# Optimization experiments

Hardware: AMD Instinct MI355X
Metric: run time of the kernel (lower is better)

## Reference

```python
import jax, jax.numpy as jnp
import numpy as np

T, B, I, H = 512, 64, 256, 256
ACT_EXP2 = 7   # activation scale = 2^-7
W_EXP2 = 8     # weight scale = 2^-8
QMIN, QMAX = -128.0, 127.0  # int8 symmetric, zp=0


def fq(x, exp2_inv):
    """Fake-quantize (round/clamp/dequant) with straight-through estimator."""
    scale = 2.0 ** (-exp2_inv)
    y = jnp.clip(jnp.round(x / scale), QMIN, QMAX) * scale
    return x + jax.lax.stop_gradient(y - x)


def setup_inputs() -> dict:
    key = jax.random.key(0)
    k = jax.random.split(key, 5)
    x = jax.random.normal(k[0], (T, B, I), jnp.float32)
    h0 = jnp.zeros((B, H), jnp.float32)
    W = jax.random.normal(k[1], (I, 3 * H), jnp.float32) / np.sqrt(I)
    R = jax.random.normal(k[2], (H, 3 * H), jnp.float32) / np.sqrt(H)
    bx = jax.random.normal(k[3], (3 * H,), jnp.float32) * 0.1
    br = jax.random.normal(k[4], (3 * H,), jnp.float32) * 0.1
    return {"x": x, "h0": h0, "W": W, "R": R, "bx": bx, "br": br}


def gru_quant(x, h0, W, R, bx, br):
    # quantize weights/biases once (weight.W / weight.R / weight.bx / weight.br)
    Wq = fq(W, W_EXP2)
    Rq = fq(R, W_EXP2)
    bxq = fq(bx, W_EXP2)
    brq = fq(br, W_EXP2)
    # hoisted input matmul: Wx = fq(fq(x) @ Wq)  -> [T, B, 3H]
    Wx = fq(jnp.einsum('tbi,ij->tbj', fq(x, ACT_EXP2), Wq), ACT_EXP2)
    Hh = h0.shape[-1]
    bz, brg, bg = bxq[:Hh], bxq[Hh:2 * Hh], bxq[2 * Hh:]

    def step(h, wx_t):
        hq = fq(h, ACT_EXP2)                      # input.h
        Rh = fq(hq @ Rq, ACT_EXP2)                # matmul.Rh
        v = fq(Rh + brq, ACT_EXP2)                # op.Rh_add_br
        wz, wr, wg = wx_t[:, :Hh], wx_t[:, Hh:2 * Hh], wx_t[:, 2 * Hh:]
        vz, vr, vg = v[:, :Hh], v[:, Hh:2 * Hh], v[:, 2 * Hh:]
        z = fq(jax.nn.sigmoid(fq(wz + bz + vz, ACT_EXP2)), ACT_EXP2)  # gate.z
        r = fq(jax.nn.sigmoid(fq(wr + brg + vr, ACT_EXP2)), ACT_EXP2)  # gate.r
        rRh = fq(r * vg, ACT_EXP2)                # op.rRh
        g = fq(jnp.tanh(fq(wg + bg + rRh, ACT_EXP2)), ACT_EXP2)        # gate.g
        old = fq(z * h, ACT_EXP2)                 # op.old_contrib
        new = fq((1.0 - z) * g, ACT_EXP2)         # op.new_contrib
        h_new = old + new
        return h_new, h_new

    _, hs = jax.lax.scan(step, h0, Wx)  # hs: [T, B, H]
    return hs


def reference(x, h0, W, R, bx, br):
    return gru_quant(x, h0, W, R, bx, br)
```

## Files before the change

### kernel.cpp

```cpp
#include <hip/hip_runtime.h>
#include <hip/hip_bf16.h>
#include <stdint.h>


#define T_STEPS 512
#define BATCH   64
#define IDIM    256
#define HDIM    256
#define N3H     768

#if defined(__has_builtin)
#if __has_builtin(__builtin_amdgcn_sdot4)
#define DOT4(a,b,c) __builtin_amdgcn_sdot4((int)(a),(int)(b),(int)(c),false)
#endif
#endif
#ifndef DOT4
__device__ __forceinline__ int dot4_sw(uint32_t a, uint32_t b, int c){
  c += (int)(int8_t)(a)      * (int)(int8_t)(b);
  c += (int)(int8_t)(a>>8)   * (int)(int8_t)(b>>8);
  c += (int)(int8_t)(a>>16)  * (int)(int8_t)(b>>16);
  c += (int)(int8_t)(a>>24)  * (int)(int8_t)(b>>24);
  return c;
}
#define DOT4(a,b,c) dot4_sw((uint32_t)(a),(uint32_t)(b),(int)(c))
#endif

#define CHUNK(W,c) (((c)&3)==0 ? W[(c)>>2].x : ((c)&3)==1 ? W[(c)>>2].y : \
                    ((c)&3)==2 ? W[(c)>>2].z : W[(c)>>2].w)

__device__ __forceinline__ int rneclamp(float v) {
  int q = (int)rintf(v);
  return min(127, max(-128, q));
}

__device__ __forceinline__ uint32_t packq4(float4 f, float sc) {
  uint32_t b0 = (uint32_t)(uint8_t)(int8_t)rneclamp(f.x * sc);
  uint32_t b1 = (uint32_t)(uint8_t)(int8_t)rneclamp(f.y * sc);
  uint32_t b2 = (uint32_t)(uint8_t)(int8_t)rneclamp(f.z * sc);
  uint32_t b3 = (uint32_t)(uint8_t)(int8_t)rneclamp(f.w * sc);
  return b0 | (b1 << 8) | (b2 << 16) | (b3 << 24);
}

__global__ void prep_kernel(const float* __restrict__ W, const float* __restrict__ R,
                            const float* __restrict__ bx, const float* __restrict__ br,
                            int8_t* __restrict__ Wq, int8_t* __restrict__ Rq,
                            int8_t* __restrict__ bx8, int8_t* __restrict__ br8) {
  const int NW = IDIM * N3H;
  int idx = blockIdx.x * 256 + threadIdx.x;
  if (idx < NW) {
    int k = idx / N3H, j = idx % N3H;
    Wq[((size_t)(k >> 4) * N3H + j) * 16 + (k & 15)] = (int8_t)rneclamp(W[idx] * 256.0f);
  } else if (idx < 2 * NW) {
    int i2 = idx - NW;
    int k = i2 / N3H, j = i2 % N3H;
    Rq[((size_t)(k >> 4) * N3H + j) * 16 + (k & 15)] = (int8_t)rneclamp(R[i2] * 256.0f);
  } else if (idx < 2 * NW + N3H) {
    int i2 = idx - 2 * NW;
    bx8[i2] = (int8_t)rneclamp(bx[i2] * 256.0f);
  } else if (idx < 2 * NW + 2 * N3H) {
    int i2 = idx - 2 * NW - N3H;
    br8[i2] = (int8_t)rneclamp(br[i2] * 256.0f);
  }
}

__global__ __launch_bounds__(768, 1) void gemm_wx_kernel(
    const float* __restrict__ x, const int8_t* __restrict__ Wq,
    int8_t* __restrict__ WxQ8) {
  const int t = blockIdx.x;
  const int j = threadIdx.x;

  __shared__ uint4 xq4[64 * 16];
  uint32_t* xq = (uint32_t*)xq4;

  uint4 w[16];
  const uint4* wp = (const uint4*)Wq;
  #pragma unroll
  for (int kk = 0; kk < 16; ++kk) w[kk] = wp[kk * N3H + j];

  const float4* xg = (const float4*)(x) + (size_t)t * 4096;
  for (int i = j; i < 4096; i += 768) {
    float4 f = xg[i];
    xq[i] = packq4(f, 128.0f);
  }
  __syncthreads();

  for (int r = 0; r < 64; ++r) {
    int s = 0;
    #pragma unroll
    for (int kk = 0; kk < 16; ++kk) {
      uint4 hv = xq4[r * 16 + kk];
      s = DOT4(hv.x, w[kk].x, s);
      s = DOT4(hv.y, w[kk].y, s);
      s = DOT4(hv.z, w[kk].z, s);
      s = DOT4(hv.w, w[kk].w, s);
    }
    int q = rneclamp((float)s * (1.0f / 256.0f));
    WxQ8[((size_t)r * T_STEPS + t) * N3H + j] = (int8_t)q;
  }
}

__global__ __launch_bounds__(256, 1) void gru_rec2_kernel(
    const float* __restrict__ h0, const int8_t* __restrict__ Rq,
    const int8_t* __restrict__ bx8, const int8_t* __restrict__ br8,
    const int8_t* __restrict__ WxQ8, float* __restrict__ out) {
  const int b = blockIdx.x;
  const int j = threadIdx.x;
  const int lane = j & 63;

  __shared__ uint32_t hq[2][64];
  __shared__ int8_t lutS[256];
  __shared__ int8_t lutT[256];

  uint4 wz[16], wr[16], wg[16];
  const uint4* rp = (const uint4*)Rq;
  #pragma unroll
  for (int kk = 0; kk < 16; ++kk) {
    wz[kk] = rp[kk * N3H + j];
    wr[kk] = rp[kk * N3H + 256 + j];
    wg[kk] = rp[kk * N3H + 512 + j];
  }
  const int bz  = (int)bx8[j];
  const int brg = (int)bx8[j + 256];
  const int bg  = (int)bx8[j + 512];
  const int vbz = (int)br8[j];
  const int vbr = (int)br8[j + 256];
  const int vbg = (int)br8[j + 512];

  {
    double a = ((double)j - 128.0) / 128.0;
    lutS[j] = (int8_t)min(127, max(-128, (int)rint(128.0 / (1.0 + exp(-a)))));
    lutT[j] = (int8_t)min(127, max(-128, (int)rint(128.0 * tanh(a))));
  }
  float hf = h0[b * HDIM + j];
  ((int8_t*)&hq[0][0])[j] = (int8_t)rneclamp(hf * 128.0f);
  __syncthreads();

  const int8_t* wxp = WxQ8 + (size_t)b * T_STEPS * N3H + j;
  float* outp = out + (size_t)b * HDIM + j;

  int wxz = (int)wxp[0];
  int wxr = (int)wxp[256];
  int wxg = (int)wxp[512];

  for (int t = 0; t < T_STEPS; ++t) {
    const int cur = t & 1, nxt = cur ^ 1;
    int nz = 0, nr = 0, ng = 0;
    if (t + 1 < T_STEPS) {
      const int8_t* p = wxp + (size_t)(t + 1) * N3H;
      nz = (int)p[0]; nr = (int)p[256]; ng = (int)p[512];
    }

    uint32_t hw = hq[cur][lane];
    int sz = 0, sr = 0, sg = 0;
    #pragma unroll
    for (int c = 0; c < 64; ++c) {
      int hc = __builtin_amdgcn_readlane((int)hw, c);
      sz = DOT4(hc, CHUNK(wz, c), sz);
      sr = DOT4(hc, CHUNK(wr, c), sr);
      sg = DOT4(hc, CHUNK(wg, c), sg);
    }
    int Rz = rneclamp((float)sz * (1.0f / 256.0f));
    int Rr = rneclamp((float)sr * (1.0f / 256.0f));
    int Rg = rneclamp((float)sg * (1.0f / 256.0f));
    int vz = rneclamp((float)(2 * Rz + vbz) * 0.5f);
    int vr = rneclamp((float)(2 * Rr + vbr) * 0.5f);
    int vg = rneclamp((float)(2 * Rg + vbg) * 0.5f);

    int az = rneclamp((float)(2 * wxz + bz + 2 * vz) * 0.5f);
    int zi = (int)lutS[az + 128];
    int ar = rneclamp((float)(2 * wxr + brg + 2 * vr) * 0.5f);
    int ri = (int)lutS[ar + 128];
    int rrh = rneclamp((float)(ri * vg) * (1.0f / 128.0f));
    int ag = rneclamp((float)(2 * wxg + bg + 2 * rrh) * 0.5f);
    int gi = (int)lutT[ag + 128];
    int oldi = rneclamp((float)zi * hf);
    int newi = rneclamp((float)((128 - zi) * gi) * (1.0f / 128.0f));
    int hi = oldi + newi;
    hf = (float)hi * (1.0f / 128.0f);
    outp[(size_t)t * BATCH * HDIM] = hf;
    ((int8_t*)&hq[nxt][0])[j] = (int8_t)min(127, max(-128, hi));
    __syncthreads();

    wxz = nz; wxr = nr; wxg = ng;
  }
}

extern "C" void kernel_launch(void* const* d_in, const int* in_sizes, int n_in,
                              void* d_out, int out_size, void* d_ws, size_t ws_size,
                              hipStream_t stream) {
  const float* x  = (const float*)d_in[0];
  const float* h0 = (const float*)d_in[1];
  const float* W  = (const float*)d_in[2];
  const float* R  = (const float*)d_in[3];
  const float* bx = (const float*)d_in[4];
  const float* br = (const float*)d_in[5];
  float* out = (float*)d_out;

  const size_t NW = (size_t)IDIM * N3H;
  int8_t* Wq  = (int8_t*)d_ws;
  int8_t* Rq  = Wq + NW;
  int8_t* bx8 = Rq + NW;
  int8_t* br8 = bx8 + N3H;
  int8_t* WxQ8 = br8 + N3H;

  {
    int total = (int)(2 * NW + 2 * N3H);
    int blocks = (total + 255) / 256;
    prep_kernel<<<blocks, 256, 0, stream>>>(W, R, bx, br, Wq, Rq, bx8, br8);
  }
  gemm_wx_kernel<<<T_STEPS, 768, 0, stream>>>(x, Wq, WxQ8);
  gru_rec2_kernel<<<BATCH, 256, 0, stream>>>(h0, Rq, bx8, br8, WxQ8, out);
}
```

Before: 488.8 us.

## Split recurrent matvec K dimension across two thread halves with shared-memory reduction

```diff
diff --git a/kernel.cpp b/kernel.cpp
--- a/kernel.cpp
+++ b/kernel.cpp
@@ -53,7 +53,7 @@
   } else if (idx < 2 * NW) {
     int i2 = idx - NW;
     int k = i2 / N3H, j = i2 % N3H;
-    Rq[((size_t)(k >> 4) * N3H + j) * 16 + (k & 15)] = (int8_t)rneclamp(R[i2] * 256.0f);
+    Rq[(size_t)j * HDIM + k] = (int8_t)rneclamp(R[i2] * 256.0f);
   } else if (idx < 2 * NW + N3H) {
     int i2 = idx - 2 * NW;
     bx8[i2] = (int8_t)rneclamp(bx[i2] * 256.0f);
@@ -99,89 +99,100 @@
   }
 }
 
-__global__ __launch_bounds__(256, 1) void gru_rec2_kernel(
+__global__ __launch_bounds__(512, 2) void gru_rec3_kernel(
     const float* __restrict__ h0, const int8_t* __restrict__ Rq,
     const int8_t* __restrict__ bx8, const int8_t* __restrict__ br8,
     const int8_t* __restrict__ WxQ8, float* __restrict__ out) {
-  const int b = blockIdx.x;
-  const int j = threadIdx.x;
-  const int lane = j & 63;
+  const int b    = blockIdx.x;
+  const int tid  = threadIdx.x;
+  const int lane = tid & 63;
+  const int half = tid >> 8;
+  const int j    = tid & 255;
 
   __shared__ uint32_t hq[2][64];
+  __shared__ int part[N3H];
   __shared__ int8_t lutS[256];
   __shared__ int8_t lutT[256];
 
-  uint4 wz[16], wr[16], wg[16];
-  const uint4* rp = (const uint4*)Rq;
-  #pragma unroll
-  for (int kk = 0; kk < 16; ++kk) {
-    wz[kk] = rp[kk * N3H + j];
-    wr[kk] = rp[kk * N3H + 256 + j];
-    wg[kk] = rp[kk * N3H + 512 + j];
-  }
-  const int bz  = (int)bx8[j];
-  const int brg = (int)bx8[j + 256];
-  const int bg  = (int)bx8[j + 512];
-  const int vbz = (int)br8[j];
-  const int vbr = (int)br8[j + 256];
-  const int vbg = (int)br8[j + 512];
-
+  uint4 wz[8], wr[8], wg[8];
   {
+    const uint4* pz = (const uint4*)(Rq + (size_t)j * HDIM)         + half * 8;
+    const uint4* pr = (const uint4*)(Rq + (size_t)(j + 256) * HDIM) + half * 8;
+    const uint4* pg = (const uint4*)(Rq + (size_t)(j + 512) * HDIM) + half * 8;
+    #pragma unroll
+    for (int kk = 0; kk < 8; ++kk) { wz[kk] = pz[kk]; wr[kk] = pr[kk]; wg[kk] = pg[kk]; }
+  }
+
+  float hf = 0.0f;
+  int bz = 0, brg = 0, bg = 0, vbz = 0, vbr = 0, vbg = 0;
+  const int8_t* wxp = WxQ8 + (size_t)b * T_STEPS * N3H + j;
+  int wxA0 = 0, wxA1 = 0, wxA2 = 0;
+  int wxB0 = 0, wxB1 = 0, wxB2 = 0;
+  if (!half) {
+    bz  = (int)bx8[j];
+    brg = (int)bx8[j + 256];
+    bg  = (int)bx8[j + 512];
+    vbz = (int)br8[j];
+    vbr = (int)br8[j + 256];
+    vbg = (int)br8[j + 512];
     double a = ((double)j - 128.0) / 128.0;
     lutS[j] = (int8_t)min(127, max(-128, (int)rint(128.0 / (1.0 + exp(-a)))));
     lutT[j] = (int8_t)min(127, max(-128, (int)rint(128.0 * tanh(a))));
-  }
-  float hf = h0[b * HDIM + j];
-  ((int8_t*)&hq[0][0])[j] = (int8_t)rneclamp(hf * 128.0f);
+    hf = h0[b * HDIM + j];
+    ((int8_t*)&hq[0][0])[j] = (int8_t)rneclamp(hf * 128.0f);
+    wxA0 = (int)wxp[0];   wxA1 = (int)wxp[256];        wxA2 = (int)wxp[512];
+    wxB0 = (int)wxp[N3H]; wxB1 = (int)wxp[N3H + 256];  wxB2 = (int)wxp[N3H + 512];
+  }
   __syncthreads();
 
-  const int8_t* wxp = WxQ8 + (size_t)b * T_STEPS * N3H + j;
   float* outp = out + (size_t)b * HDIM + j;
-
-  int wxz = (int)wxp[0];
-  int wxr = (int)wxp[256];
-  int wxg = (int)wxp[512];
 
   for (int t = 0; t < T_STEPS; ++t) {
     const int cur = t & 1, nxt = cur ^ 1;
+
     int nz = 0, nr = 0, ng = 0;
-    if (t + 1 < T_STEPS) {
-      const int8_t* p = wxp + (size_t)(t + 1) * N3H;
+    if (!half) {
+      const int8_t* p = wxp + (size_t)min(t + 2, T_STEPS - 1) * N3H;
       nz = (int)p[0]; nr = (int)p[256]; ng = (int)p[512];
     }
 
-    uint32_t hw = hq[cur][lane];
+    uint32_t hw = hq[cur][half * 32 + (lane & 31)];
     int sz = 0, sr = 0, sg = 0;
     #pragma unroll
-    for (int c = 0; c < 64; ++c) {
+    for (int c = 0; c < 32; ++c) {
       int hc = __builtin_amdgcn_readlane((int)hw, c);
       sz = DOT4(hc, CHUNK(wz, c), sz);
       sr = DOT4(hc, CHUNK(wr, c), sr);
       sg = DOT4(hc, CHUNK(wg, c), sg);
     }
-    int Rz = rneclamp((float)sz * (1.0f / 256.0f));
-    int Rr = rneclamp((float)sr * (1.0f / 256.0f));
-    int Rg = rneclamp((float)sg * (1.0f / 256.0f));
-    int vz = rneclamp((float)(2 * Rz + vbz) * 0.5f);
-    int vr = rneclamp((float)(2 * Rr + vbr) * 0.5f);
-    int vg = rneclamp((float)(2 * Rg + vbg) * 0.5f);
-
-    int az = rneclamp((float)(2 * wxz + bz + 2 * vz) * 0.5f);
-    int zi = (int)lutS[az + 128];
-    int ar = rneclamp((float)(2 * wxr + brg + 2 * vr) * 0.5f);
-    int ri = (int)lutS[ar + 128];
-    int rrh = rneclamp((float)(ri * vg) * (1.0f / 128.0f));
-    int ag = rneclamp((float)(2 * wxg + bg + 2 * rrh) * 0.5f);
-    int gi = (int)lutT[ag + 128];
-    int oldi = rneclamp((float)zi * hf);
-    int newi = rneclamp((float)((128 - zi) * gi) * (1.0f / 128.0f));
-    int hi = oldi + newi;
-    hf = (float)hi * (1.0f / 128.0f);
-    outp[(size_t)t * BATCH * HDIM] = hf;
-    ((int8_t*)&hq[nxt][0])[j] = (int8_t)min(127, max(-128, hi));
+    if (half) { part[j] = sz; part[j + 256] = sr; part[j + 512] = sg; }
     __syncthreads();
 
-    wxz = nz; wxr = nr; wxg = ng;
+    if (!half) {
+      sz += part[j]; sr += part[j + 256]; sg += part[j + 512];
+      int Rz = rneclamp((float)sz * (1.0f / 256.0f));
+      int Rr = rneclamp((float)sr * (1.0f / 256.0f));
+      int Rg = rneclamp((float)sg * (1.0f / 256.0f));
+      int vz = rneclamp((float)(2 * Rz + vbz) * 0.5f);
+      int vr = rneclamp((float)(2 * Rr + vbr) * 0.5f);
+      int vg = rneclamp((float)(2 * Rg + vbg) * 0.5f);
+      int az = rneclamp((float)(2 * wxA0 + bz + 2 * vz) * 0.5f);
+      int zi = (int)lutS[az + 128];
+      int ar = rneclamp((float)(2 * wxA1 + brg + 2 * vr) * 0.5f);
+      int ri = (int)lutS[ar + 128];
+      int rrh = rneclamp((float)(ri * vg) * (1.0f / 128.0f));
+      int ag = rneclamp((float)(2 * wxA2 + bg + 2 * rrh) * 0.5f);
+      int gi = (int)lutT[ag + 128];
+      int oldi = rneclamp((float)zi * hf);
+      int newi = rneclamp((float)((128 - zi) * gi) * (1.0f / 128.0f));
+      int hi = oldi + newi;
+      hf = (float)hi * (1.0f / 128.0f);
+      outp[(size_t)t * BATCH * HDIM] = hf;
+      ((int8_t*)&hq[nxt][0])[j] = (int8_t)min(127, max(-128, hi));
+      wxA0 = wxB0; wxA1 = wxB1; wxA2 = wxB2;
+      wxB0 = nz;   wxB1 = nr;   wxB2 = ng;
+    }
+    __syncthreads();
   }
 }
 
@@ -209,5 +220,5 @@
     prep_kernel<<<blocks, 256, 0, stream>>>(W, R, bx, br, Wq, Rq, bx8, br8);
   }
   gemm_wx_kernel<<<T_STEPS, 768, 0, stream>>>(x, Wq, WxQ8);
-  gru_rec2_kernel<<<BATCH, 256, 0, stream>>>(h0, Rq, bx8, br8, WxQ8, out);
-}
+  gru_rec3_kernel<<<BATCH, 512, 0, stream>>>(h0, Rq, bx8, br8, WxQ8, out);
+}
```

New measurement: 555.0 us. 13.5% more time.
